# Kernel tuning notes

Measured on AMD Instinct MI355X. Metric: run time of the kernel, lower is better.

The kernel has to match this reference:

```python
import jax, jax.numpy as jnp
import numpy as np

D_MODEL = 2048
NUM_HEADS = 16
D_K = D_MODEL // NUM_HEADS
B, S, PAST = 2, 1024, 3072


def setup_inputs() -> dict:
    key = jax.random.key(0)
    ks = jax.random.split(key, 12)
    s = 1.0 / np.sqrt(D_MODEL)
    inp = {
        "x": jax.random.normal(ks[0], (B, S, D_MODEL), dtype=jnp.float32),
        "past_key": jax.random.normal(ks[1], (B, NUM_HEADS, PAST, D_K), dtype=jnp.float32),
        "past_value": jax.random.normal(ks[2], (B, NUM_HEADS, PAST, D_K), dtype=jnp.float32),
        "Wq": jax.random.normal(ks[3], (D_MODEL, D_MODEL), dtype=jnp.float32) * s,
        "bq": jax.random.normal(ks[4], (D_MODEL,), dtype=jnp.float32) * s,
        "Wk": jax.random.normal(ks[5], (D_MODEL, D_MODEL), dtype=jnp.float32) * s,
        "bk": jax.random.normal(ks[6], (D_MODEL,), dtype=jnp.float32) * s,
        "Wv": jax.random.normal(ks[7], (D_MODEL, D_MODEL), dtype=jnp.float32) * s,
        "bv": jax.random.normal(ks[8], (D_MODEL,), dtype=jnp.float32) * s,
        "Wo": jax.random.normal(ks[9], (D_MODEL, D_MODEL), dtype=jnp.float32) * s,
        "bo": jax.random.normal(ks[10], (D_MODEL,), dtype=jnp.float32) * s,
    }
    return inp


def reference(x, past_key, past_value, Wq, bq, Wk, bk, Wv, bv, Wo, bo):
    b, s, _ = x.shape
    # torch nn.Linear: y = x @ W^T + b
    def proj(W, bias):
        y = jnp.einsum('bsd,ed->bse', x, W) + bias
        return y.reshape(b, s, NUM_HEADS, D_K).transpose(0, 2, 1, 3)  # [B,H,S,dk]
    Q = proj(Wq, bq)
    K = proj(Wk, bk)
    V = proj(Wv, bv)
    K = jnp.concatenate([past_key, K], axis=2)   # [B,H,PAST+S,dk]
    V = jnp.concatenate([past_value, V], axis=2)
    scale = 1.0 / np.sqrt(D_K).astype(np.float32)
    scores = jnp.einsum('bhqd,bhkd->bhqk', Q, K) * scale
    attn = jax.nn.softmax(scores, axis=-1)
    out = jnp.einsum('bhqk,bhkd->bhqd', attn, V)          # [B,H,S,dk]
    out = out.transpose(0, 2, 1, 3).reshape(b, s, D_MODEL)
    out = jnp.einsum('bsd,ed->bse', out, Wo) + bo
    return out, K, V
```

## Files before the change

### kernel.cpp

```cpp
#include <hip/hip_runtime.h>
#include <stdint.h>

typedef __bf16 bf16;
typedef __bf16 bf16x4 __attribute__((ext_vector_type(4)));
typedef __bf16 bf16x8 __attribute__((ext_vector_type(8)));
typedef float  f32x4  __attribute__((ext_vector_type(4)));

#define DMODEL 2048
#define NH 16
#define DK 128
#define SS 1024
#define PASTLEN 3072
#define LTOT 4096
#define KVTILES 64
#define NSPLIT 4
#define NT 16

__device__ __forceinline__ void gload16(const void* g, void* l) {
    __builtin_amdgcn_global_load_lds(
        (__attribute__((address_space(1))) void*)(uintptr_t)g,
        (__attribute__((address_space(3))) void*)(uintptr_t)l,
        16, 0, 0);
}

__global__ __launch_bounds__(256) void cvt5_k(
    const float* __restrict__ s0, const float* __restrict__ s1,
    const float* __restrict__ s2, const float* __restrict__ s3,
    const float* __restrict__ s4,
    bf16* __restrict__ d0, bf16* __restrict__ d1, bf16* __restrict__ d2,
    bf16* __restrict__ d3, bf16* __restrict__ d4, int n8)
{
    const float* s; bf16* d;
    switch (blockIdx.y) {
        case 0: s = s0; d = d0; break;
        case 1: s = s1; d = d1; break;
        case 2: s = s2; d = d2; break;
        case 3: s = s3; d = d3; break;
        default: s = s4; d = d4; break;
    }
    int stride = gridDim.x * blockDim.x;
    for (int i = blockIdx.x*blockDim.x + threadIdx.x; i < n8; i += stride) {
        const float4* p = (const float4*)s + (size_t)i*2;
        float4 a = p[0], b = p[1];
        bf16x8 o;
        o[0]=(bf16)a.x; o[1]=(bf16)a.y; o[2]=(bf16)a.z; o[3]=(bf16)a.w;
        o[4]=(bf16)b.x; o[5]=(bf16)b.y; o[6]=(bf16)b.z; o[7]=(bf16)b.w;
        *((bf16x8*)d + i) = o;
    }
}

__global__ __launch_bounds__(256) void gemm_bt(
    const bf16* __restrict__ A,
    const bf16* __restrict__ W0, const bf16* __restrict__ W1, const bf16* __restrict__ W2,
    const float* __restrict__ b0, const float* __restrict__ b1, const float* __restrict__ b2,
    bf16* __restrict__ outQ, float* __restrict__ outK, float* __restrict__ outV,
    float* __restrict__ outO, int mode)
{
    __shared__ __align__(16) bf16 As[128*32];
    __shared__ __align__(16) bf16 Bs[128*32];
    const int tid  = threadIdx.x;
    const int wave = tid >> 6, lane = tid & 63;
    const int l15 = lane & 15, l4 = lane >> 4;
    int which, ntile;
    if (mode == 0) { which = blockIdx.y >> 4; ntile = blockIdx.y & 15; }
    else           { which = 3;               ntile = blockIdx.y; }
    const bf16*  W    = (mode != 0 || which == 0) ? W0 : (which == 1 ? W1 : W2);
    const float* bias = (mode != 0 || which == 0) ? b0 : (which == 1 ? b1 : b2);
    const int m0 = blockIdx.x * 128, n0 = ntile * 128;
    const int wm = wave >> 1, wn = wave & 1;

    f32x4 acc[4][4] = {};

    for (int k0 = 0; k0 < DMODEL; k0 += 32) {
        __syncthreads();
        #pragma unroll
        for (int c = 0; c < 2; ++c) {
            const int base = c*4096 + wave*1024;
            const int byte = base + lane*16;
            const int row  = byte >> 6;
            const int ke   = (byte & 63) >> 1;
            gload16(A + (size_t)(m0+row)*DMODEL + k0 + ke, (char*)As + base);
            gload16(W + (size_t)(n0+row)*DMODEL + k0 + ke, (char*)Bs + base);
        }
        asm volatile("s_waitcnt vmcnt(0)" ::: "memory");
        __syncthreads();
        bf16x8 af[4], bfv[4];
        #pragma unroll
        for (int mf = 0; mf < 4; ++mf)
            af[mf] = *(const bf16x8*)((const char*)As + (wm*64 + mf*16 + l15)*64 + l4*16);
        #pragma unroll
        for (int nf = 0; nf < 4; ++nf)
            bfv[nf] = *(const bf16x8*)((const char*)Bs + (wn*64 + nf*16 + l15)*64 + l4*16);
        #pragma unroll
        for (int mf = 0; mf < 4; ++mf)
            #pragma unroll
            for (int nf = 0; nf < 4; ++nf)
                acc[mf][nf] = __builtin_amdgcn_mfma_f32_16x16x32_bf16(af[mf], bfv[nf], acc[mf][nf], 0, 0, 0);
    }

    float bv4[4];
    #pragma unroll
    for (int nf = 0; nf < 4; ++nf) bv4[nf] = bias[n0 + wn*64 + nf*16 + l15];

    const int rbase = m0 + wm*64 + l4*4;
    const int cbase = n0 + wn*64 + l15;

    if (mode == 1) {
        #pragma unroll
        for (int mf = 0; mf < 4; ++mf)
        #pragma unroll
        for (int nf = 0; nf < 4; ++nf) {
            const int col = cbase + nf*16;
            #pragma unroll
            for (int r = 0; r < 4; ++r) {
                const int row = rbase + mf*16 + r;
                outO[(size_t)row*DMODEL + col] = acc[mf][nf][r] + bv4[nf];
            }
        }
    } else if (which == 0) {
        const float qs = 0.08838834764831845f * 1.4426950408889634f;
        #pragma unroll
        for (int mf = 0; mf < 4; ++mf)
        #pragma unroll
        for (int nf = 0; nf < 4; ++nf) {
            const int col = cbase + nf*16;
            const int h = col >> 7, d = col & 127;
            #pragma unroll
            for (int r = 0; r < 4; ++r) {
                const int row = rbase + mf*16 + r;
                const int b = row >> 10, s = row & 1023;
                outQ[((size_t)(b*NH + h)*SS + s)*DK + d] = (bf16)((acc[mf][nf][r] + bv4[nf]) * qs);
            }
        }
    } else {
        float* dst = (which == 1) ? outK : outV;
        #pragma unroll
        for (int mf = 0; mf < 4; ++mf)
        #pragma unroll
        for (int nf = 0; nf < 4; ++nf) {
            const int col = cbase + nf*16;
            const int h = col >> 7, d = col & 127;
            #pragma unroll
            for (int r = 0; r < 4; ++r) {
                const int row = rbase + mf*16 + r;
                const int b = row >> 10, s = row & 1023;
                dst[((size_t)(b*NH + h)*LTOT + PASTLEN + s)*DK + d] = acc[mf][nf][r] + bv4[nf];
            }
        }
    }
}

__global__ __launch_bounds__(256) void kvprep_k(
    const float* __restrict__ pk, const float* __restrict__ pv,
    float* __restrict__ Kf, float* __restrict__ Vf,
    bf16* __restrict__ Kb, bf16* __restrict__ Vb)
{
    __shared__ float Vt_f[64*132];
    const int tid = threadIdx.x;
    const int tau = blockIdx.x, bh = blockIdx.y;
    const bool past = tau < 48;
    const size_t srcoff = past ? ((size_t)bh*PASTLEN + tau*64)*DK
                               : ((size_t)bh*LTOT    + tau*64)*DK;
    const float* srcK = (past ? pk : Kf) + srcoff;
    const float* srcV = (past ? pv : Vf) + srcoff;
    float* dstKf = Kf + ((size_t)bh*LTOT + tau*64)*DK;
    float* dstVf = Vf + ((size_t)bh*LTOT + tau*64)*DK;
    char* kblob = (char*)Kb + (((size_t)bh*KVTILES + tau) << 14);
    char* vblob = (char*)Vb + (((size_t)bh*KVTILES + tau) << 14);

    #pragma unroll
    for (int i = 0; i < 8; ++i) {
        const int f4 = i*256 + tid;
        const int r  = f4 >> 5;
        const int c8 = f4 & 31;
        float4 k4 = ((const float4*)srcK)[f4];
        float4 v4 = ((const float4*)srcV)[f4];
        if (past) {
            ((float4*)dstKf)[f4] = k4;
            ((float4*)dstVf)[f4] = v4;
        }
        bf16x4 kq; kq[0]=(bf16)k4.x; kq[1]=(bf16)k4.y; kq[2]=(bf16)k4.z; kq[3]=(bf16)k4.w;
        *(bf16x4*)(kblob + r*256 + ((c8*8) ^ ((r&7)<<4))) = kq;
        *(float4*)&Vt_f[r*132 + c8*4] = v4;
    }
    __syncthreads();
    const int d = tid >> 1, half = tid & 1;
    const int dx = (d & 7) << 4;
    #pragma unroll
    for (int jj = 0; jj < 4; ++jj) {
        const int chunk = half*4 + jj;
        bf16x8 o;
        #pragma unroll
        for (int e = 0; e < 8; ++e) {
            const int j  = chunk*8 + e;
            const int oe = (j & 32) + ((j & 4) << 2) + (((j >> 3) & 3) << 2) + (j & 3);
            o[e] = (bf16)Vt_f[oe*132 + d];
        }
        *(bf16x8*)(vblob + d*128 + ((chunk*16) ^ dx)) = o;
    }
}

__global__ __launch_bounds__(512, 2) void attn_k(
    const bf16* __restrict__ Qb,
    const bf16* __restrict__ Kb, const bf16* __restrict__ Vb,
    bf16* __restrict__ Opart, float* __restrict__ Marr, float* __restrict__ Larr)
{
    __shared__ __align__(16) char KL[4][16384];
    __shared__ __align__(16) char VL[4][16384];

    const int tid  = threadIdx.x;
    const int wave = tid >> 6, lane = tid & 63;
    const int l15 = lane & 15, l4 = lane >> 4;
    const int wgid = blockIdx.x;
    const int qt = (wgid >> 3) & 3;
    const int g  = ((wgid >> 5) << 3) | (wgid & 7);
    const int bh = g >> 2, sp = g & 3;
    const int qbase = qt*256 + wave*32;

    bf16x8 qf[2][4];
    #pragma unroll
    for (int qq = 0; qq < 2; ++qq) {
        const bf16* qptr = Qb + ((size_t)bh*SS + qbase + qq*16 + l15)*DK;
        #pragma unroll
        for (int ks = 0; ks < 4; ++ks)
            qf[qq][ks] = *(const bf16x8*)(qptr + ks*32 + l4*8);
    }

    const char* kblobs = (const char*)Kb + (((size_t)bh*KVTILES + sp*NT) << 14);
    const char* vblobs = (const char*)Vb + (((size_t)bh*KVTILES + sp*NT) << 14);
    const int soff = wave*2048;

    bf16x8 ones8;
    #pragma unroll
    for (int e = 0; e < 8; ++e) ones8[e] = (bf16)1.0f;

    float m_run[2];
    f32x4 oacc[2][8];
    f32x4 lacc[2];
    m_run[0] = -1e30f; m_run[1] = -1e30f;
    #pragma unroll
    for (int qq = 0; qq < 2; ++qq) {
        #pragma unroll
        for (int df = 0; df < 8; ++df) oacc[qq][df] = f32x4{0.f,0.f,0.f,0.f};
        lacc[qq] = f32x4{0.f,0.f,0.f,0.f};
    }

    #pragma unroll
    for (int tt = 0; tt < 2; ++tt)
        #pragma unroll
        for (int c = 0; c < 2; ++c) {
            gload16(kblobs + ((size_t)tt << 14) + soff + c*1024 + lane*16, KL[tt] + soff + c*1024);
            gload16(vblobs + ((size_t)tt << 14) + soff + c*1024 + lane*16, VL[tt] + soff + c*1024);
        }

    for (int t = 0; t < NT; ++t) {
        const int cur = t & 3;
        if (t + 2 < NT) {
            const int nb = (t + 2) & 3;
            const char* kb = kblobs + ((size_t)(t+2) << 14);
            const char* vb = vblobs + ((size_t)(t+2) << 14);
            #pragma unroll
            for (int c = 0; c < 2; ++c) {
                gload16(kb + soff + c*1024 + lane*16, KL[nb] + soff + c*1024);
                gload16(vb + soff + c*1024 + lane*16, VL[nb] + soff + c*1024);
            }
            asm volatile("s_waitcnt vmcnt(8)" ::: "memory");
        } else if (t + 1 < NT) {
            asm volatile("s_waitcnt vmcnt(4)" ::: "memory");
        } else {
            asm volatile("s_waitcnt vmcnt(0)" ::: "memory");
        }
        __builtin_amdgcn_s_barrier();

        const char* Kc = KL[cur];
        const char* Vc = VL[cur];

        f32x4 sa[2][4];
        #pragma unroll
        for (int qq = 0; qq < 2; ++qq)
            #pragma unroll
            for (int nf = 0; nf < 4; ++nf) sa[qq][nf] = f32x4{0.f,0.f,0.f,0.f};
        __builtin_amdgcn_s_setprio(1);
        #pragma unroll
        for (int nf = 0; nf < 4; ++nf) {
            const int krow = nf*16 + l15;
            const int rx = (krow & 7) << 4;
            #pragma unroll
            for (int ks = 0; ks < 4; ++ks) {
                bf16x8 kf = *(const bf16x8*)(Kc + krow*256 + ((ks*64 + l4*16) ^ rx));
                sa[0][nf] = __builtin_amdgcn_mfma_f32_16x16x32_bf16(kf, qf[0][ks], sa[0][nf], 0,0,0);
                sa[1][nf] = __builtin_amdgcn_mfma_f32_16x16x32_bf16(kf, qf[1][ks], sa[1][nf], 0,0,0);
            }
        }
        __builtin_amdgcn_s_setprio(0);

        float mt2[2];
        #pragma unroll
        for (int qq = 0; qq < 2; ++qq) {
            float a0 = fmaxf(fmaxf(sa[qq][0][0], sa[qq][0][1]), fmaxf(sa[qq][0][2], sa[qq][0][3]));
            float a1 = fmaxf(fmaxf(sa[qq][1][0], sa[qq][1][1]), fmaxf(sa[qq][1][2], sa[qq][1][3]));
            float a2 = fmaxf(fmaxf(sa[qq][2][0], sa[qq][2][1]), fmaxf(sa[qq][2][2], sa[qq][2][3]));
            float a3 = fmaxf(fmaxf(sa[qq][3][0], sa[qq][3][1]), fmaxf(sa[qq][3][2], sa[qq][3][3]));
            float v = fmaxf(fmaxf(a0, a1), fmaxf(a2, a3));
            v = fmaxf(v, __shfl_xor(v, 16, 64));
            v = fmaxf(v, __shfl_xor(v, 32, 64));
            mt2[qq] = v;
        }
        const bool ok = (mt2[0] <= m_run[0] + 8.0f) && (mt2[1] <= m_run[1] + 8.0f);
        if (!__all(ok)) {
            #pragma unroll
            for (int qq = 0; qq < 2; ++qq) {
                const float mn   = fmaxf(m_run[qq], mt2[qq]);
                const float corr = exp2f(m_run[qq] - mn);
                m_run[qq] = mn;
                #pragma unroll
                for (int r = 0; r < 4; ++r) {
                    const float c = __shfl(corr, (lane & 48) | (l4*4 + r), 64);
                    lacc[qq][r] *= c;
                    #pragma unroll
                    for (int df = 0; df < 8; ++df) oacc[qq][df][r] *= c;
                }
            }
        }

        bf16x8 pf[2][2];
        #pragma unroll
        for (int qq = 0; qq < 2; ++qq)
            #pragma unroll
            for (int ks2 = 0; ks2 < 2; ++ks2) {
                bf16x8 v;
                #pragma unroll
                for (int e = 0; e < 8; ++e)
                    v[e] = (bf16)exp2f(sa[qq][ks2*2 + (e >> 2)][e & 3] - m_run[qq]);
                pf[qq][ks2] = v;
            }

        __builtin_amdgcn_s_setprio(1);
        #pragma unroll
        for (int ks2 = 0; ks2 < 2; ++ks2) {
            lacc[0] = __builtin_amdgcn_mfma_f32_16x16x32_bf16(pf[0][ks2], ones8, lacc[0], 0,0,0);
            lacc[1] = __builtin_amdgcn_mfma_f32_16x16x32_bf16(pf[1][ks2], ones8, lacc[1], 0,0,0);
            #pragma unroll
            for (int df = 0; df < 8; ++df) {
                const int d = df*16 + l15;
                bf16x8 vf = *(const bf16x8*)(Vc + d*128 + ((ks2*64 + l4*16) ^ ((d&7)<<4)));
                oacc[0][df] = __builtin_amdgcn_mfma_f32_16x16x32_bf16(pf[0][ks2], vf, oacc[0][df], 0,0,0);
                oacc[1][df] = __builtin_amdgcn_mfma_f32_16x16x32_bf16(pf[1][ks2], vf, oacc[1][df], 0,0,0);
            }
        }
        __builtin_amdgcn_s_setprio(0);
    }

    bf16* op = Opart + ((size_t)sp*32 + bh)*SS*DK;
    #pragma unroll
    for (int qq = 0; qq < 2; ++qq)
        #pragma unroll
        for (int df = 0; df < 8; ++df)
            #pragma unroll
            for (int r = 0; r < 4; ++r) {
                const int q = qbase + qq*16 + l4*4 + r;
                op[(size_t)q*DK + df*16 + l15] = (bf16)oacc[qq][df][r];
            }
    if (l4 == 0) {
        #pragma unroll
        for (int qq = 0; qq < 2; ++qq)
            Marr[(size_t)sp*32768 + bh*SS + qbase + qq*16 + l15] = m_run[qq];
    }
    if (l15 == 0) {
        #pragma unroll
        for (int qq = 0; qq < 2; ++qq)
            #pragma unroll
            for (int r = 0; r < 4; ++r) {
                const int q = qbase + qq*16 + l4*4 + r;
                Larr[(size_t)sp*32768 + bh*SS + q] = lacc[qq][r];
            }
    }
}

__global__ __launch_bounds__(256) void combine_k(
    const bf16* __restrict__ Opart, const float* __restrict__ Marr,
    const float* __restrict__ Larr, bf16* __restrict__ Ob)
{
    const int gid = blockIdx.x*256 + threadIdx.x;
    const int row = gid >> 4;
    const int c8  = gid & 15;
    const int bh = row >> 10, q = row & 1023;
    float m[NSPLIT], l[NSPLIT];
    #pragma unroll
    for (int s = 0; s < NSPLIT; ++s) {
        m[s] = Marr[(size_t)s*32768 + row];
        l[s] = Larr[(size_t)s*32768 + row];
    }
    float M = m[0];
    #pragma unroll
    for (int s = 1; s < NSPLIT; ++s) M = fmaxf(M, m[s]);
    float w[NSPLIT], den = 0.f;
    #pragma unroll
    for (int s = 0; s < NSPLIT; ++s) { w[s] = exp2f(m[s] - M); den += l[s]*w[s]; }
    const float inv = 1.f / den;
    #pragma unroll
    for (int s = 0; s < NSPLIT; ++s) w[s] *= inv;
    float acc[8] = {};
    #pragma unroll
    for (int s = 0; s < NSPLIT; ++s) {
        bf16x8 p = *(const bf16x8*)(Opart + (size_t)s*4194304 + (size_t)row*DK + c8*8);
        #pragma unroll
        for (int e = 0; e < 8; ++e) acc[e] += (float)p[e]*w[s];
    }
    const int b = bh >> 4, h = bh & 15;
    bf16x8 o;
    #pragma unroll
    for (int e = 0; e < 8; ++e) o[e] = (bf16)acc[e];
    *(bf16x8*)(Ob + ((size_t)(b*SS + q))*DMODEL + h*DK + c8*8) = o;
}

extern "C" void kernel_launch(void* const* d_in, const int* in_sizes, int n_in,
                              void* d_out, int out_size, void* d_ws, size_t ws_size,
                              hipStream_t stream) {
    const float* x  = (const float*)d_in[0];
    const float* pk = (const float*)d_in[1];
    const float* pv = (const float*)d_in[2];
    const float* Wq = (const float*)d_in[3];
    const float* bq = (const float*)d_in[4];
    const float* Wk = (const float*)d_in[5];
    const float* bk = (const float*)d_in[6];
    const float* Wv = (const float*)d_in[7];
    const float* bv = (const float*)d_in[8];
    const float* Wo = (const float*)d_in[9];
    const float* bo = (const float*)d_in[10];

    float* out  = (float*)d_out;
    float* Kout = out + 4194304;
    float* Vout = out + 20971520;

    char* ws = (char*)d_ws;
    bf16* xb    = (bf16*)(ws);
    bf16* Wqb   = (bf16*)(ws + (size_t)8*1024*1024);
    bf16* Wkb   = (bf16*)(ws + (size_t)16*1024*1024);
    bf16* Wvb   = (bf16*)(ws + (size_t)24*1024*1024);
    bf16* Wob   = (bf16*)(ws + (size_t)32*1024*1024);
    bf16* Qb    = (bf16*)(ws + (size_t)40*1024*1024);
    bf16* Ob    = (bf16*)(ws + (size_t)48*1024*1024);
    bf16* Kb    = (bf16*)(ws + (size_t)56*1024*1024);
    bf16* Vb    = (bf16*)(ws + (size_t)88*1024*1024);
    bf16*  Opart = (bf16*)(ws);
    float* Marr  = out;
    float* Larr  = out + 131072;

    cvt5_k<<<dim3(1024, 5), 256, 0, stream>>>(x, Wq, Wk, Wv, Wo,
                                              xb, Wqb, Wkb, Wvb, Wob, 524288);
    gemm_bt<<<dim3(16, 48), 256, 0, stream>>>(xb, Wqb, Wkb, Wvb, bq, bk, bv,
                                              Qb, Kout, Vout, nullptr, 0);
    kvprep_k<<<dim3(64, 32), 256, 0, stream>>>(pk, pv, Kout, Vout, Kb, Vb);
    attn_k<<<512, 512, 0, stream>>>(Qb, Kb, Vb, Opart, Marr, Larr);
    combine_k<<<2048, 256, 0, stream>>>(Opart, Marr, Larr, Ob);
    gemm_bt<<<dim3(16, 16), 256, 0, stream>>>(Ob, Wob, nullptr, nullptr, bo, nullptr, nullptr,
                                              nullptr, nullptr, nullptr, out, 1);
}
```

Baseline: 286.8 us.

## Switch attention kernel to 32x32x16 MFMA with transposed score layout

Rewrites the attention inner loop to use 32x32x16 bf16 MFMAs, with each lane owning one query row. This makes the row max and row sum mostly lane-local, and the row sum now comes from scalar adds instead of a ones-vector MFMA. P is packed into bf16 with v_cvt_pk_bf16_f32 and v_permlane32_swap instead of per-element conversion, and the V blob layout is simplified to match the new fragment order. It adds an extra barrier per tile and depends on the permlane swap producing the correct fragment ordering.

Measured after the change: 297.8 us. 3.8% more time.

```diff
diff --git a/kernel.cpp b/kernel.cpp
--- a/kernel.cpp
+++ b/kernel.cpp
@@ -5,6 +5,7 @@
 typedef __bf16 bf16x4 __attribute__((ext_vector_type(4)));
 typedef __bf16 bf16x8 __attribute__((ext_vector_type(8)));
 typedef float  f32x4  __attribute__((ext_vector_type(4)));
+typedef float  f32x16 __attribute__((ext_vector_type(16)));
 
 #define DMODEL 2048
 #define NH 16
@@ -21,6 +22,15 @@
         (__attribute__((address_space(1))) void*)(uintptr_t)g,
         (__attribute__((address_space(3))) void*)(uintptr_t)l,
         16, 0, 0);
+}
+
+__device__ __forceinline__ uint32_t cvtpk(float a, float b) {
+    uint32_t r;
+    asm("v_cvt_pk_bf16_f32 %0, %1, %2" : "=v"(r) : "v"(a), "v"(b));
+    return r;
+}
+__device__ __forceinline__ void pswap(uint32_t& a, uint32_t& b) {
+    asm volatile("v_permlane32_swap_b32 %0, %1" : "+v"(a), "+v"(b));
 }
 
 __global__ __launch_bounds__(256) void cvt5_k(
@@ -191,11 +201,8 @@
         const int chunk = half*4 + jj;
         bf16x8 o;
         #pragma unroll
-        for (int e = 0; e < 8; ++e) {
-            const int j  = chunk*8 + e;
-            const int oe = (j & 32) + ((j & 4) << 2) + (((j >> 3) & 3) << 2) + (j & 3);
-            o[e] = (bf16)Vt_f[oe*132 + d];
-        }
+        for (int e = 0; e < 8; ++e)
+            o[e] = (bf16)Vt_f[(chunk*8 + e)*132 + d];
         *(bf16x8*)(vblob + d*128 + ((chunk*16) ^ dx)) = o;
     }
 }
@@ -210,40 +217,28 @@
 
     const int tid  = threadIdx.x;
     const int wave = tid >> 6, lane = tid & 63;
-    const int l15 = lane & 15, l4 = lane >> 4;
+    const int l31 = lane & 31, hi = lane >> 5;
     const int wgid = blockIdx.x;
     const int qt = (wgid >> 3) & 3;
     const int g  = ((wgid >> 5) << 3) | (wgid & 7);
     const int bh = g >> 2, sp = g & 3;
-    const int qbase = qt*256 + wave*32;
-
-    bf16x8 qf[2][4];
-    #pragma unroll
-    for (int qq = 0; qq < 2; ++qq) {
-        const bf16* qptr = Qb + ((size_t)bh*SS + qbase + qq*16 + l15)*DK;
-        #pragma unroll
-        for (int ks = 0; ks < 4; ++ks)
-            qf[qq][ks] = *(const bf16x8*)(qptr + ks*32 + l4*8);
+    const int q  = qt*256 + wave*32 + l31;
+
+    bf16x8 qf[8];
+    {
+        const bf16* qptr = Qb + ((size_t)bh*SS + q)*DK;
+        #pragma unroll
+        for (int ks = 0; ks < 8; ++ks)
+            qf[ks] = *(const bf16x8*)(qptr + ks*16 + hi*8);
     }
 
     const char* kblobs = (const char*)Kb + (((size_t)bh*KVTILES + sp*NT) << 14);
     const char* vblobs = (const char*)Vb + (((size_t)bh*KVTILES + sp*NT) << 14);
     const int soff = wave*2048;
-
-    bf16x8 ones8;
-    #pragma unroll
-    for (int e = 0; e < 8; ++e) ones8[e] = (bf16)1.0f;
-
-    float m_run[2];
-    f32x4 oacc[2][8];
-    f32x4 lacc[2];
-    m_run[0] = -1e30f; m_run[1] = -1e30f;
-    #pragma unroll
-    for (int qq = 0; qq < 2; ++qq) {
-        #pragma unroll
-        for (int df = 0; df < 8; ++df) oacc[qq][df] = f32x4{0.f,0.f,0.f,0.f};
-        lacc[qq] = f32x4{0.f,0.f,0.f,0.f};
-    }
+    const int kswz = (l31 & 7) << 4;
+
+    float m_run = -1e30f, l_run = 0.f;
+    f32x16 oacc[4] = {};
 
     #pragma unroll
     for (int tt = 0; tt < 2; ++tt)
@@ -275,105 +270,104 @@
         const char* Kc = KL[cur];
         const char* Vc = VL[cur];
 
-        f32x4 sa[2][4];
-        #pragma unroll
-        for (int qq = 0; qq < 2; ++qq)
-            #pragma unroll
-            for (int nf = 0; nf < 4; ++nf) sa[qq][nf] = f32x4{0.f,0.f,0.f,0.f};
+        f32x16 sa0 = {}, sa1 = {};
         __builtin_amdgcn_s_setprio(1);
         #pragma unroll
-        for (int nf = 0; nf < 4; ++nf) {
-            const int krow = nf*16 + l15;
-            const int rx = (krow & 7) << 4;
-            #pragma unroll
-            for (int ks = 0; ks < 4; ++ks) {
-                bf16x8 kf = *(const bf16x8*)(Kc + krow*256 + ((ks*64 + l4*16) ^ rx));
-                sa[0][nf] = __builtin_amdgcn_mfma_f32_16x16x32_bf16(kf, qf[0][ks], sa[0][nf], 0,0,0);
-                sa[1][nf] = __builtin_amdgcn_mfma_f32_16x16x32_bf16(kf, qf[1][ks], sa[1][nf], 0,0,0);
-            }
+        for (int ks = 0; ks < 8; ++ks) {
+            const int koff = (ks*32 + hi*16) ^ kswz;
+            bf16x8 kf0 = *(const bf16x8*)(Kc + l31*256 + koff);
+            bf16x8 kf1 = *(const bf16x8*)(Kc + (32 + l31)*256 + koff);
+            sa0 = __builtin_amdgcn_mfma_f32_32x32x16_bf16(kf0, qf[ks], sa0, 0, 0, 0);
+            sa1 = __builtin_amdgcn_mfma_f32_32x32x16_bf16(kf1, qf[ks], sa1, 0, 0, 0);
         }
         __builtin_amdgcn_s_setprio(0);
 
-        float mt2[2];
-        #pragma unroll
-        for (int qq = 0; qq < 2; ++qq) {
-            float a0 = fmaxf(fmaxf(sa[qq][0][0], sa[qq][0][1]), fmaxf(sa[qq][0][2], sa[qq][0][3]));
-            float a1 = fmaxf(fmaxf(sa[qq][1][0], sa[qq][1][1]), fmaxf(sa[qq][1][2], sa[qq][1][3]));
-            float a2 = fmaxf(fmaxf(sa[qq][2][0], sa[qq][2][1]), fmaxf(sa[qq][2][2], sa[qq][2][3]));
-            float a3 = fmaxf(fmaxf(sa[qq][3][0], sa[qq][3][1]), fmaxf(sa[qq][3][2], sa[qq][3][3]));
-            float v = fmaxf(fmaxf(a0, a1), fmaxf(a2, a3));
-            v = fmaxf(v, __shfl_xor(v, 16, 64));
-            v = fmaxf(v, __shfl_xor(v, 32, 64));
-            mt2[qq] = v;
-        }
-        const bool ok = (mt2[0] <= m_run[0] + 8.0f) && (mt2[1] <= m_run[1] + 8.0f);
+        float v16[16];
+        #pragma unroll
+        for (int e = 0; e < 16; ++e) v16[e] = fmaxf(sa0[e], sa1[e]);
+        #pragma unroll
+        for (int st = 8; st > 0; st >>= 1)
+            #pragma unroll
+            for (int e = 0; e < 8; ++e)
+                if (e < st) v16[e] = fmaxf(v16[e], v16[e + st]);
+        float mt = v16[0];
+        mt = fmaxf(mt, __shfl_xor(mt, 32, 64));
+
+        const bool ok = (mt <= m_run + 8.0f);
         if (!__all(ok)) {
-            #pragma unroll
-            for (int qq = 0; qq < 2; ++qq) {
-                const float mn   = fmaxf(m_run[qq], mt2[qq]);
-                const float corr = exp2f(m_run[qq] - mn);
-                m_run[qq] = mn;
+            const float mn   = fmaxf(m_run, mt);
+            const float corr = exp2f(m_run - mn);
+            m_run = mn;
+            l_run *= corr;
+            #pragma unroll
+            for (int db = 0; db < 4; ++db)
                 #pragma unroll
-                for (int r = 0; r < 4; ++r) {
-                    const float c = __shfl(corr, (lane & 48) | (l4*4 + r), 64);
-                    lacc[qq][r] *= c;
-                    #pragma unroll
-                    for (int df = 0; df < 8; ++df) oacc[qq][df][r] *= c;
-                }
-            }
-        }
-
-        bf16x8 pf[2][2];
-        #pragma unroll
-        for (int qq = 0; qq < 2; ++qq)
-            #pragma unroll
-            for (int ks2 = 0; ks2 < 2; ++ks2) {
-                bf16x8 v;
+                for (int e = 0; e < 16; ++e) oacc[db][e] *= corr;
+        }
+
+        float p0[16], p1[16];
+        #pragma unroll
+        for (int e = 0; e < 16; ++e) {
+            p0[e] = exp2f(sa0[e] - m_run);
+            p1[e] = exp2f(sa1[e] - m_run);
+        }
+        {
+            float s16[16];
+            #pragma unroll
+            for (int e = 0; e < 16; ++e) s16[e] = p0[e] + p1[e];
+            #pragma unroll
+            for (int st = 8; st > 0; st >>= 1)
                 #pragma unroll
                 for (int e = 0; e < 8; ++e)
-                    v[e] = (bf16)exp2f(sa[qq][ks2*2 + (e >> 2)][e & 3] - m_run[qq]);
-                pf[qq][ks2] = v;
+                    if (e < st) s16[e] += s16[e + st];
+            float s = s16[0];
+            s += __shfl_xor(s, 32, 64);
+            l_run += s;
+        }
+
+        union U8 { uint32_t w[4]; bf16x8 v; };
+        bf16x8 pf[4];
+        #pragma unroll
+        for (int s4 = 0; s4 < 4; ++s4) {
+            const float* P = (s4 < 2) ? (p0 + (s4 & 1)*8) : (p1 + (s4 & 1)*8);
+            uint32_t a = cvtpk(P[0], P[1]);
+            uint32_t b = cvtpk(P[4], P[5]);
+            uint32_t c = cvtpk(P[2], P[3]);
+            uint32_t d = cvtpk(P[6], P[7]);
+            pswap(a, b);
+            pswap(c, d);
+            U8 u; u.w[0] = a; u.w[1] = c; u.w[2] = b; u.w[3] = d;
+            pf[s4] = u.v;
+        }
+
+        __builtin_amdgcn_s_setprio(1);
+        #pragma unroll
+        for (int db = 0; db < 4; ++db) {
+            const int drow = db*32 + l31;
+            #pragma unroll
+            for (int kvs = 0; kvs < 4; ++kvs) {
+                bf16x8 vf = *(const bf16x8*)(Vc + drow*128 + ((kvs*32 + hi*16) ^ kswz));
+                oacc[db] = __builtin_amdgcn_mfma_f32_32x32x16_bf16(vf, pf[kvs], oacc[db], 0, 0, 0);
             }
-
-        __builtin_amdgcn_s_setprio(1);
-        #pragma unroll
-        for (int ks2 = 0; ks2 < 2; ++ks2) {
-            lacc[0] = __builtin_amdgcn_mfma_f32_16x16x32_bf16(pf[0][ks2], ones8, lacc[0], 0,0,0);
-            lacc[1] = __builtin_amdgcn_mfma_f32_16x16x32_bf16(pf[1][ks2], ones8, lacc[1], 0,0,0);
-            #pragma unroll
-            for (int df = 0; df < 8; ++df) {
-                const int d = df*16 + l15;
-                bf16x8 vf = *(const bf16x8*)(Vc + d*128 + ((ks2*64 + l4*16) ^ ((d&7)<<4)));
-                oacc[0][df] = __builtin_amdgcn_mfma_f32_16x16x32_bf16(pf[0][ks2], vf, oacc[0][df], 0,0,0);
-                oacc[1][df] = __builtin_amdgcn_mfma_f32_16x16x32_bf16(pf[1][ks2], vf, oacc[1][df], 0,0,0);
-            }
         }
         __builtin_amdgcn_s_setprio(0);
-    }
-
-    bf16* op = Opart + ((size_t)sp*32 + bh)*SS*DK;
-    #pragma unroll
-    for (int qq = 0; qq < 2; ++qq)
-        #pragma unroll
-        for (int df = 0; df < 8; ++df)
-            #pragma unroll
-            for (int r = 0; r < 4; ++r) {
-                const int q = qbase + qq*16 + l4*4 + r;
-                op[(size_t)q*DK + df*16 + l15] = (bf16)oacc[qq][df][r];
-            }
-    if (l4 == 0) {
-        #pragma unroll
-        for (int qq = 0; qq < 2; ++qq)
-            Marr[(size_t)sp*32768 + bh*SS + qbase + qq*16 + l15] = m_run[qq];
-    }
-    if (l15 == 0) {
-        #pragma unroll
-        for (int qq = 0; qq < 2; ++qq)
-            #pragma unroll
-            for (int r = 0; r < 4; ++r) {
-                const int q = qbase + qq*16 + l4*4 + r;
-                Larr[(size_t)sp*32768 + bh*SS + q] = lacc[qq][r];
-            }
+
+        __builtin_amdgcn_s_barrier();
+    }
+
+    bf16* op = Opart + ((size_t)sp*32 + bh)*SS*DK + (size_t)q*DK;
+    #pragma unroll
+    for (int db = 0; db < 4; ++db)
+        #pragma unroll
+        for (int rq = 0; rq < 4; ++rq) {
+            bf16x4 o4;
+            #pragma unroll
+            for (int i = 0; i < 4; ++i) o4[i] = (bf16)oacc[db][rq*4 + i];
+            *(bf16x4*)(op + db*32 + rq*8 + hi*4) = o4;
+        }
+    if (hi == 0) {
+        Marr[(size_t)sp*32768 + bh*SS + q] = m_run;
+        Larr[(size_t)sp*32768 + bh*SS + q] = l_run;
     }
 }
 
```
